# Optimization experiments

Hardware: AMD Instinct MI355X
Metric: run time of the kernel (lower is better)

## Reference

```python
import jax, jax.numpy as jnp
import numpy as np

EMBED = 1024
HEADS = 16
HEAD_DIM = EMBED // HEADS


def setup_inputs() -> dict:
    key = jax.random.key(0)
    ks = jax.random.split(key, 12)
    N, S, E = 4, 2048, EMBED
    scale = 1.0 / np.sqrt(E)
    inp = {
        "values": jax.random.normal(ks[0], (N, S, E), dtype=jnp.float32),
        "keys": jax.random.normal(ks[1], (N, S, E), dtype=jnp.float32),
        "query": jax.random.normal(ks[2], (N, S, E), dtype=jnp.float32),
        "mask": jnp.ones((N, 1, 1, S), dtype=jnp.int32),
        # Linear params: y = x @ W + b (W stored as [in, out])
        "Wv": jax.random.normal(ks[3], (E, E), dtype=jnp.float32) * scale,
        "bv": jnp.zeros((E,), dtype=jnp.float32),
        "Wk": jax.random.normal(ks[4], (E, E), dtype=jnp.float32) * scale,
        "bk": jnp.zeros((E,), dtype=jnp.float32),
        "Wq": jax.random.normal(ks[5], (E, E), dtype=jnp.float32) * scale,
        "bq": jnp.zeros((E,), dtype=jnp.float32),
        "Wo": jax.random.normal(ks[6], (E, E), dtype=jnp.float32) * scale,
        "bo": jnp.zeros((E,), dtype=jnp.float32),
    }
    return inp


def reference(values, keys, query, mask, Wv, bv, Wk, bk, Wq, bq, Wo, bo):
    N, Q, E = query.shape
    V = values.shape[1]
    K = keys.shape[1]
    v = (values @ Wv + bv).reshape(N, V, HEADS, HEAD_DIM)
    k = (keys @ Wk + bk).reshape(N, K, HEADS, HEAD_DIM)
    q = (query @ Wq + bq).reshape(N, Q, HEADS, HEAD_DIM)
    # energy: [N, H, Q, K]
    energy = jnp.einsum("nqhd,nkhd->nhqk", q, k)
    energy = jnp.where(mask == 0, jnp.float32(-1e20), energy)
    # NOTE: original scales by sqrt(embed_size), not sqrt(head_dim)
    attn = jax.nn.softmax(energy / jnp.sqrt(jnp.float32(E)), axis=3)
    out = jnp.einsum("nhql,nlhd->nqhd", attn, v).reshape(N, Q, E)
    return out @ Wo + bo
```

## Files before the change

kernel.cpp:

```cpp
#include <hip/hip_runtime.h>

#define H 16
#define DH 64
#define S 2048
#define E 1024
#define NB 4

typedef short short8_t __attribute__((ext_vector_type(8)));
typedef short short4_t __attribute__((ext_vector_type(4)));
typedef float float4_t __attribute__((ext_vector_type(4)));

__device__ inline unsigned short f2bf(float f) {
    union { float f; unsigned u; } v; v.f = f;
    unsigned r = v.u + 0x7fffu + ((v.u >> 16) & 1u);
    return (unsigned short)(r >> 16);
}

__device__ __forceinline__ unsigned pk_bf16(float a, float b) {
    union { float f; unsigned u; } ua, ub;
    ua.f = a; ub.f = b;
    unsigned ra = ua.u + 0x7fffu + ((ua.u >> 16) & 1u);
    unsigned rb = ub.u + 0x7fffu + ((ub.u >> 16) & 1u);
    return __builtin_amdgcn_perm(rb, ra, 0x07060302u);
}

__device__ __forceinline__ unsigned cvt_pk_bf16(float a, float b) {
    unsigned r;
    asm("v_cvt_pk_bf16_f32 %0, %1, %2" : "=v"(r) : "v"(a), "v"(b));
    return r;
}

__device__ __forceinline__ float4_t mfma16x16x16_bf16(short4_t a, short4_t b, float4_t c) {
#if __has_builtin(__builtin_amdgcn_mfma_f32_16x16x16bf16_1k)
    return __builtin_amdgcn_mfma_f32_16x16x16bf16_1k(a, b, c, 0, 0, 0);
#else
    float4_t d;
    asm("v_mfma_f32_16x16x16_bf16 %0, %1, %2, %3" : "=v"(d) : "v"(a), "v"(b), "v"(c));
    return d;
#endif
}

__device__ __forceinline__ void async_copy16(const unsigned short* g, unsigned short* l) {
    __builtin_amdgcn_global_load_lds(
        (const __attribute__((address_space(1))) unsigned int*)g,
        (__attribute__((address_space(3))) unsigned int*)l, 16, 0, 0);
}

__global__ __launch_bounds__(256) void xcvt_kernel(
    const float* __restrict__ v, const float* __restrict__ k,
    const float* __restrict__ q, unsigned short* __restrict__ xv,
    unsigned short* __restrict__ xk, unsigned short* __restrict__ xq)
{
    const int z = blockIdx.y;
    const float* src = (z == 0) ? v : (z == 1) ? k : q;
    unsigned short* dst = (z == 0) ? xv : (z == 1) ? xk : xq;
    size_t i0 = ((size_t)blockIdx.x * 256 + threadIdx.x) * 8;
    float4 f0 = *reinterpret_cast<const float4*>(src + i0);
    float4 f1 = *reinterpret_cast<const float4*>(src + i0 + 4);
    uint4 o;
    o.x = pk_bf16(f0.x, f0.y); o.y = pk_bf16(f0.z, f0.w);
    o.z = pk_bf16(f1.x, f1.y); o.w = pk_bf16(f1.z, f1.w);
    *reinterpret_cast<uint4*>(dst + i0) = o;
}

__global__ __launch_bounds__(256) void wcvt_kernel(
    const float* __restrict__ Wv, const float* __restrict__ Wk,
    const float* __restrict__ Wq, const float* __restrict__ Wo,
    unsigned short* __restrict__ Wt)
{
    __shared__ float tile[64][65];
    const float* W = (blockIdx.z == 0) ? Wv : (blockIdx.z == 1) ? Wk
                   : (blockIdx.z == 2) ? Wq : Wo;
    unsigned short* out = Wt + (size_t)blockIdx.z * (E * E);
    const int k0 = blockIdx.x * 64, n0 = blockIdx.y * 64;
    const int tid = threadIdx.x;
#pragma unroll
    for (int i = 0; i < 4; ++i) {
        int c = i * 256 + tid;
        int kl = c >> 4, nl4 = (c & 15) * 4;
        float4 v = *reinterpret_cast<const float4*>(W + (size_t)(k0 + kl) * E + n0 + nl4);
        tile[kl][nl4 + 0] = v.x; tile[kl][nl4 + 1] = v.y;
        tile[kl][nl4 + 2] = v.z; tile[kl][nl4 + 3] = v.w;
    }
    __syncthreads();
#pragma unroll
    for (int i = 0; i < 4; ++i) {
        int c = i * 256 + tid;
        int nl = c >> 4, kl4 = (c & 15) * 4;
        ushort4 o;
        o.x = f2bf(tile[kl4 + 0][nl]); o.y = f2bf(tile[kl4 + 1][nl]);
        o.z = f2bf(tile[kl4 + 2][nl]); o.w = f2bf(tile[kl4 + 3][nl]);
        *reinterpret_cast<ushort4*>(out + (size_t)(n0 + nl) * E + k0 + kl4) = o;
    }
}

__global__ __launch_bounds__(256) void proj_kernel(
    const unsigned short* __restrict__ A, const unsigned short* __restrict__ WT,
    const float* __restrict__ bias, unsigned short* __restrict__ out, int mode)
{
    __shared__ __align__(16) unsigned short As[2][128][64];
    __shared__ __align__(16) unsigned short Bs[2][128][64];

    const int tid = threadIdx.x;
    const int m0 = blockIdx.y * 128;
    const int n0 = blockIdx.x * 128;
    const int wave = tid >> 6, lane = tid & 63;
    const int wm = wave >> 1, wn = wave & 1;
    const int quad = lane >> 4, l16 = lane & 15;
    const int r8 = lane >> 3;
    const int c8 = (lane & 7) ^ (r8 & 7);

    float4_t acc[4][4];
#pragma unroll
    for (int i = 0; i < 4; ++i)
#pragma unroll
        for (int j = 0; j < 4; ++j) { float4_t z = {0.f,0.f,0.f,0.f}; acc[i][j] = z; }

#pragma unroll
    for (int j = 0; j < 4; ++j) {
        int row = wave * 32 + j * 8 + r8;
        async_copy16(A  + (size_t)(m0 + row) * E + c8 * 8, &As[0][wave * 32 + j * 8][0]);
        async_copy16(WT + (size_t)(n0 + row) * E + c8 * 8, &Bs[0][wave * 32 + j * 8][0]);
    }

    for (int it = 0; it < 16; ++it) {
        const int cur = it & 1, nxt = cur ^ 1;
        __syncthreads();

        if (it < 15) {
            const int kn = (it + 1) * 64;
#pragma unroll
            for (int j = 0; j < 4; ++j) {
                int row = wave * 32 + j * 8 + r8;
                async_copy16(A  + (size_t)(m0 + row) * E + kn + c8 * 8, &As[nxt][wave * 32 + j * 8][0]);
                async_copy16(WT + (size_t)(n0 + row) * E + kn + c8 * 8, &Bs[nxt][wave * 32 + j * 8][0]);
            }
        }
#pragma unroll
        for (int kk = 0; kk < 2; ++kk) {
            short8_t a[4], b[4];
#pragma unroll
            for (int mi = 0; mi < 4; ++mi)
                a[mi] = *reinterpret_cast<const short8_t*>(
                    &As[cur][wm * 64 + mi * 16 + l16][((kk * 4 + quad) ^ (l16 & 7)) * 8]);
#pragma unroll
            for (int nj = 0; nj < 4; ++nj)
                b[nj] = *reinterpret_cast<const short8_t*>(
                    &Bs[cur][wn * 64 + nj * 16 + l16][((kk * 4 + quad) ^ (l16 & 7)) * 8]);
#pragma unroll
            for (int mi = 0; mi < 4; ++mi)
#pragma unroll
                for (int nj = 0; nj < 4; ++nj)
                    acc[mi][nj] = __builtin_amdgcn_mfma_f32_16x16x32_bf16(a[mi], b[nj], acc[mi][nj], 0, 0, 0);
        }
    }
#pragma unroll
    for (int mi = 0; mi < 4; ++mi) {
#pragma unroll
        for (int nj = 0; nj < 4; ++nj) {
            int gcol = n0 + wn * 64 + nj * 16 + l16;
            float bvv = bias[gcol];
            int h = gcol >> 6, d = gcol & 63;
#pragma unroll
            for (int r = 0; r < 4; ++r) {
                int gm = m0 + wm * 64 + mi * 16 + quad * 4 + r;
                float val = acc[mi][nj][r] + bvv;
                int n = gm >> 11, s = gm & 2047;
                size_t addr;
                if (mode == 0)
                    addr = (((size_t)(n * H + h)) * DH + d) * S + s;
                else
                    addr = (((size_t)(n * H + h)) * S + s) * DH + d;
                out[addr] = f2bf(val);
            }
        }
    }
}

__global__ __launch_bounds__(256, 4) void flash_kernel(
    const unsigned short* __restrict__ Qb, const unsigned short* __restrict__ Kb,
    const unsigned short* __restrict__ VTb, const int* __restrict__ mask,
    unsigned short* __restrict__ AO)
{
    __shared__ __align__(16) unsigned short Ks[2][64][64];
    __shared__ __align__(16) unsigned short Vs[2][64][64];
    __shared__ float am[2][64];
    __shared__ float lbuf[4][32];

    const int tid = threadIdx.x;
    const int wave = tid >> 6, lane = tid & 63;
    const int quad = lane >> 4, l16 = lane & 15;
    const int r8 = lane >> 3;
    const int c8 = (lane & 7) ^ (r8 & 7);

    const int wlin = blockIdx.y * 16 + blockIdx.x;
    const int wid = (wlin & 7) * 128 + (wlin >> 3);
    const int qt = wid & 15;
    const int nh = wid >> 4;
    const int n = nh >> 4, h = nh & 15;
    const size_t hb = (size_t)nh * S * DH;
    const unsigned short* Qh = Qb + hb;
    const unsigned short* Kh = Kb + hb;
    const unsigned short* Vh = VTb + hb;
    const int* mp = mask + n * S;

    const float c1 = 0.03125f * 1.4426950408889634f;
    const float C2_UNMASK = -23.083120654223414f;
    const float C2_MASK   = -1.44e20f;

    short8_t qa[2][2];
#pragma unroll
    for (int qb2 = 0; qb2 < 2; ++qb2)
#pragma unroll
        for (int kk = 0; kk < 2; ++kk) {
            int row = qt * 128 + wave * 32 + qb2 * 16 + l16;
            qa[qb2][kk] = *reinterpret_cast<const short8_t*>(Qh + (size_t)row * DH + kk * 32 + quad * 8);
        }

    float4_t o[2][4];
#pragma unroll
    for (int mi = 0; mi < 2; ++mi)
#pragma unroll
        for (int nj = 0; nj < 4; ++nj) { float4_t z = {0.f,0.f,0.f,0.f}; o[mi][nj] = z; }
    float lsum[2] = {0.f, 0.f};

#pragma unroll
    for (int j = 0; j < 2; ++j) {
        int row = wave * 16 + j * 8 + r8;
        async_copy16(Kh + (size_t)row * DH + c8 * 8, &Ks[0][wave * 16 + j * 8][0]);
        async_copy16(Vh + (size_t)row * S + c8 * 8,  &Vs[0][wave * 16 + j * 8][0]);
    }
    if (tid < 64) am[0][tid] = (mp[tid] == 0) ? C2_MASK : C2_UNMASK;

    for (int it = 0; it < 32; ++it) {
        const int cur = it & 1, nxt = cur ^ 1;
        __syncthreads();

        const int kn = (it < 31) ? (it + 1) * 64 : 0;
#pragma unroll
        for (int j = 0; j < 2; ++j) {
            int row = wave * 16 + j * 8 + r8;
            async_copy16(Kh + (size_t)(kn + row) * DH + c8 * 8, &Ks[nxt][wave * 16 + j * 8][0]);
            async_copy16(Vh + (size_t)row * S + kn + c8 * 8,    &Vs[nxt][wave * 16 + j * 8][0]);
        }
        if (tid < 64) am[nxt][tid] = (mp[kn + tid] == 0) ? C2_MASK : C2_UNMASK;

        float4_t st[4][2];
#pragma unroll
        for (int kvb = 0; kvb < 4; ++kvb)
#pragma unroll
            for (int qb2 = 0; qb2 < 2; ++qb2) { float4_t z = {0.f,0.f,0.f,0.f}; st[kvb][qb2] = z; }
        __builtin_amdgcn_s_setprio(1);
#pragma unroll
        for (int kk = 0; kk < 2; ++kk) {
            short8_t ak[4];
#pragma unroll
            for (int kvb = 0; kvb < 4; ++kvb)
                ak[kvb] = *reinterpret_cast<const short8_t*>(
                    &Ks[cur][kvb * 16 + l16][((kk * 4 + quad) ^ (l16 & 7)) * 8]);
#pragma unroll
            for (int kvb = 0; kvb < 4; ++kvb)
#pragma unroll
                for (int qb2 = 0; qb2 < 2; ++qb2)
                    st[kvb][qb2] = __builtin_amdgcn_mfma_f32_16x16x32_bf16(ak[kvb], qa[qb2][kk], st[kvb][qb2], 0, 0, 0);
        }
        __builtin_amdgcn_s_setprio(0);

        unsigned pw[2][4][2];
#pragma unroll
        for (int kvb = 0; kvb < 4; ++kvb) {
            float4 c2v = *reinterpret_cast<const float4*>(&am[cur][kvb * 16 + quad * 4]);
#pragma unroll
            for (int qb2 = 0; qb2 < 2; ++qb2) {
                float p0 = __builtin_amdgcn_exp2f(st[kvb][qb2][0] * c1 + c2v.x);
                float p1 = __builtin_amdgcn_exp2f(st[kvb][qb2][1] * c1 + c2v.y);
                float p2 = __builtin_amdgcn_exp2f(st[kvb][qb2][2] * c1 + c2v.z);
                float p3 = __builtin_amdgcn_exp2f(st[kvb][qb2][3] * c1 + c2v.w);
                lsum[qb2] += (p0 + p1) + (p2 + p3);
                pw[qb2][kvb][0] = cvt_pk_bf16(p0, p1);
                pw[qb2][kvb][1] = cvt_pk_bf16(p2, p3);
            }
        }

        const int vcol = (quad & 1) * 4;
        __builtin_amdgcn_s_setprio(1);
#pragma unroll
        for (int kvb = 0; kvb < 4; ++kvb) {
            const int vch = ((kvb * 2 + (quad >> 1)) ^ (l16 & 7)) * 8 + vcol;
            short4_t vb[4];
#pragma unroll
            for (int nj = 0; nj < 4; ++nj)
                vb[nj] = *reinterpret_cast<const short4_t*>(&Vs[cur][nj * 16 + l16][vch]);
#pragma unroll
            for (int mi = 0; mi < 2; ++mi) {
                union { unsigned u[2]; short4_t s; } pu;
                pu.u[0] = pw[mi][kvb][0]; pu.u[1] = pw[mi][kvb][1];
#pragma unroll
                for (int nj = 0; nj < 4; ++nj)
                    o[mi][nj] = mfma16x16x16_bf16(pu.s, vb[nj], o[mi][nj]);
            }
        }
        __builtin_amdgcn_s_setprio(0);
    }

    lsum[0] += __shfl_xor(lsum[0], 16); lsum[0] += __shfl_xor(lsum[0], 32);
    lsum[1] += __shfl_xor(lsum[1], 16); lsum[1] += __shfl_xor(lsum[1], 32);
    if (lane < 16) { lbuf[wave][lane] = lsum[0]; lbuf[wave][16 + lane] = lsum[1]; }

#pragma unroll
    for (int mi = 0; mi < 2; ++mi) {
        float4 lv = *reinterpret_cast<const float4*>(&lbuf[wave][mi * 16 + quad * 4]);
#pragma unroll
        for (int r = 0; r < 4; ++r) {
            float invl = __builtin_amdgcn_rcpf(((const float*)&lv)[r]);
            int qrow = qt * 128 + wave * 32 + mi * 16 + quad * 4 + r;
            size_t gm = (size_t)n * S + qrow;
#pragma unroll
            for (int nj = 0; nj < 4; ++nj) {
                int col = h * DH + nj * 16 + l16;
                AO[gm * E + col] = f2bf(o[mi][nj][r] * invl);
            }
        }
    }
}

__global__ __launch_bounds__(256) void ogemm_kernel(
    const unsigned short* __restrict__ A, const unsigned short* __restrict__ WT,
    const float* __restrict__ bias, float* __restrict__ out)
{
    __shared__ __align__(16) unsigned short As[2][128][64];
    __shared__ __align__(16) unsigned short Bs[2][128][64];

    const int tid = threadIdx.x;
    const int m0 = blockIdx.y * 128;
    const int n0 = blockIdx.x * 128;
    const int wave = tid >> 6, lane = tid & 63;
    const int wm = wave >> 1, wn = wave & 1;
    const int quad = lane >> 4, l16 = lane & 15;
    const int r8 = lane >> 3;
    const int c8 = (lane & 7) ^ (r8 & 7);

    float4_t acc[4][4];
#pragma unroll
    for (int i = 0; i < 4; ++i)
#pragma unroll
        for (int j = 0; j < 4; ++j) { float4_t z = {0.f,0.f,0.f,0.f}; acc[i][j] = z; }

#pragma unroll
    for (int j = 0; j < 4; ++j) {
        int row = wave * 32 + j * 8 + r8;
        async_copy16(A  + (size_t)(m0 + row) * E + c8 * 8, &As[0][wave * 32 + j * 8][0]);
        async_copy16(WT + (size_t)(n0 + row) * E + c8 * 8, &Bs[0][wave * 32 + j * 8][0]);
    }

    for (int it = 0; it < 16; ++it) {
        const int cur = it & 1, nxt = cur ^ 1;
        __syncthreads();

        if (it < 15) {
            const int kn = (it + 1) * 64;
#pragma unroll
            for (int j = 0; j < 4; ++j) {
                int row = wave * 32 + j * 8 + r8;
                async_copy16(A  + (size_t)(m0 + row) * E + kn + c8 * 8, &As[nxt][wave * 32 + j * 8][0]);
                async_copy16(WT + (size_t)(n0 + row) * E + kn + c8 * 8, &Bs[nxt][wave * 32 + j * 8][0]);
            }
        }
#pragma unroll
        for (int kk = 0; kk < 2; ++kk) {
            short8_t a[4], b[4];
#pragma unroll
            for (int mi = 0; mi < 4; ++mi)
                a[mi] = *reinterpret_cast<const short8_t*>(
                    &As[cur][wm * 64 + mi * 16 + l16][((kk * 4 + quad) ^ (l16 & 7)) * 8]);
#pragma unroll
            for (int nj = 0; nj < 4; ++nj)
                b[nj] = *reinterpret_cast<const short8_t*>(
                    &Bs[cur][wn * 64 + nj * 16 + l16][((kk * 4 + quad) ^ (l16 & 7)) * 8]);
#pragma unroll
            for (int mi = 0; mi < 4; ++mi)
#pragma unroll
                for (int nj = 0; nj < 4; ++nj)
                    acc[mi][nj] = __builtin_amdgcn_mfma_f32_16x16x32_bf16(a[mi], b[nj], acc[mi][nj], 0, 0, 0);
        }
    }
#pragma unroll
    for (int mi = 0; mi < 4; ++mi)
#pragma unroll
        for (int nj = 0; nj < 4; ++nj) {
            int gcol = n0 + wn * 64 + nj * 16 + l16;
            float bvv = bias[gcol];
#pragma unroll
            for (int r = 0; r < 4; ++r) {
                int gm = m0 + wm * 64 + mi * 16 + quad * 4 + r;
                out[(size_t)gm * E + gcol] = acc[mi][nj][r] + bvv;
            }
        }
}

extern "C" void kernel_launch(void* const* d_in, const int* in_sizes, int n_in,
                              void* d_out, int out_size, void* d_ws, size_t ws_size,
                              hipStream_t stream) {
    const float* values = (const float*)d_in[0];
    const float* keys   = (const float*)d_in[1];
    const float* query  = (const float*)d_in[2];
    const int*   mask   = (const int*)d_in[3];
    const float* Wv = (const float*)d_in[4];  const float* bv = (const float*)d_in[5];
    const float* Wk = (const float*)d_in[6];  const float* bk = (const float*)d_in[7];
    const float* Wq = (const float*)d_in[8];  const float* bq = (const float*)d_in[9];
    const float* Wo = (const float*)d_in[10]; const float* bo = (const float*)d_in[11];
    float* out = (float*)d_out;

    char* ws = (char*)d_ws;
    unsigned short* Wt = (unsigned short*)ws;
    unsigned short* xv = (unsigned short*)(ws + 8388608);
    unsigned short* xk = (unsigned short*)(ws + 25165824);
    unsigned short* xq = (unsigned short*)(ws + 41943040);
    unsigned short* vt = (unsigned short*)(ws + 58720256);
    unsigned short* kb = xv;
    unsigned short* qb = xk;
    unsigned short* ao = xq;

    xcvt_kernel<<<dim3(4096, 3), 256, 0, stream>>>(values, keys, query, xv, xk, xq);
    wcvt_kernel<<<dim3(16, 16, 4), 256, 0, stream>>>(Wv, Wk, Wq, Wo, Wt);
    proj_kernel<<<dim3(8, 64), 256, 0, stream>>>(xv, Wt,           bv, vt, 0);
    proj_kernel<<<dim3(8, 64), 256, 0, stream>>>(xk, Wt + 1048576, bk, kb, 1);
    proj_kernel<<<dim3(8, 64), 256, 0, stream>>>(xq, Wt + 2097152, bq, qb, 1);
    flash_kernel<<<dim3(16, 64), 256, 0, stream>>>(qb, kb, vt, mask, ao);
    ogemm_kernel<<<dim3(8, 64), 256, 0, stream>>>(ao, Wt + 3145728, bo, out);
}
```

Before: 377.4 us.

## Split flash blocks into eight waves and transpose V-projection MFMA for coalesced stores

The flash kernel now runs 512 threads per block. Each wave owns 16 query rows instead of 32, and K and V tile loads are split between the two halves of the block, which lowers per-wave register pressure and raises the number of waves in flight. The projection kernel is templated on mode, and for the V-transpose mode it swaps the MFMA operands so each lane holds consecutive sequence positions, making the transposed output stores more contiguous. In exchange, every K/V shared-memory tile is now reused by more waves, and each MFMA issues with a smaller per-wave tile, which may reduce per-wave compute efficiency.

Result: slower. 401.1 us (+6.3%).

```diff
diff --git a/kernel.cpp b/kernel.cpp
--- a/kernel.cpp
+++ b/kernel.cpp
@@ -94,9 +94,10 @@
     }
 }
 
+template<int MODE>
 __global__ __launch_bounds__(256) void proj_kernel(
     const unsigned short* __restrict__ A, const unsigned short* __restrict__ WT,
-    const float* __restrict__ bias, unsigned short* __restrict__ out, int mode)
+    const float* __restrict__ bias, unsigned short* __restrict__ out)
 {
     __shared__ __align__(16) unsigned short As[2][128][64];
     __shared__ __align__(16) unsigned short Bs[2][128][64];
@@ -148,36 +149,55 @@
                 b[nj] = *reinterpret_cast<const short8_t*>(
                     &Bs[cur][wn * 64 + nj * 16 + l16][((kk * 4 + quad) ^ (l16 & 7)) * 8]);
 #pragma unroll
-            for (int mi = 0; mi < 4; ++mi)
-#pragma unroll
-                for (int nj = 0; nj < 4; ++nj)
-                    acc[mi][nj] = __builtin_amdgcn_mfma_f32_16x16x32_bf16(a[mi], b[nj], acc[mi][nj], 0, 0, 0);
-        }
-    }
-#pragma unroll
-    for (int mi = 0; mi < 4; ++mi) {
-#pragma unroll
-        for (int nj = 0; nj < 4; ++nj) {
-            int gcol = n0 + wn * 64 + nj * 16 + l16;
-            float bvv = bias[gcol];
-            int h = gcol >> 6, d = gcol & 63;
-#pragma unroll
-            for (int r = 0; r < 4; ++r) {
-                int gm = m0 + wm * 64 + mi * 16 + quad * 4 + r;
-                float val = acc[mi][nj][r] + bvv;
-                int n = gm >> 11, s = gm & 2047;
-                size_t addr;
-                if (mode == 0)
-                    addr = (((size_t)(n * H + h)) * DH + d) * S + s;
-                else
-                    addr = (((size_t)(n * H + h)) * S + s) * DH + d;
-                out[addr] = f2bf(val);
+            for (int x = 0; x < 4; ++x)
+#pragma unroll
+                for (int y = 0; y < 4; ++y) {
+                    if (MODE == 0)
+                        acc[x][y] = __builtin_amdgcn_mfma_f32_16x16x32_bf16(b[x], a[y], acc[x][y], 0, 0, 0);
+                    else
+                        acc[x][y] = __builtin_amdgcn_mfma_f32_16x16x32_bf16(a[x], b[y], acc[x][y], 0, 0, 0);
+                }
+        }
+    }
+
+    if (MODE == 0) {
+#pragma unroll
+        for (int x = 0; x < 4; ++x) {
+            float4 bb = *reinterpret_cast<const float4*>(&bias[n0 + wn * 64 + x * 16 + quad * 4]);
+#pragma unroll
+            for (int y = 0; y < 4; ++y) {
+                int m = m0 + wm * 64 + y * 16 + l16;
+                int nn = m >> 11, s = m & 2047;
+#pragma unroll
+                for (int r = 0; r < 4; ++r) {
+                    int gcol = n0 + wn * 64 + x * 16 + quad * 4 + r;
+                    int h = gcol >> 6, d = gcol & 63;
+                    float val = acc[x][y][r] + ((const float*)&bb)[r];
+                    out[(((size_t)(nn * H + h)) * DH + d) * S + s] = f2bf(val);
+                }
             }
         }
-    }
-}
-
-__global__ __launch_bounds__(256, 4) void flash_kernel(
+    } else {
+#pragma unroll
+        for (int x = 0; x < 4; ++x) {
+#pragma unroll
+            for (int y = 0; y < 4; ++y) {
+                int gcol = n0 + wn * 64 + y * 16 + l16;
+                float bvv = bias[gcol];
+                int h = gcol >> 6, d = gcol & 63;
+#pragma unroll
+                for (int r = 0; r < 4; ++r) {
+                    int gm = m0 + wm * 64 + x * 16 + quad * 4 + r;
+                    float val = acc[x][y][r] + bvv;
+                    int nn = gm >> 11, s = gm & 2047;
+                    out[(((size_t)(nn * H + h)) * S + s) * DH + d] = f2bf(val);
+                }
+            }
+        }
+    }
+}
+
+__global__ __launch_bounds__(512, 8) void flash_kernel(
     const unsigned short* __restrict__ Qb, const unsigned short* __restrict__ Kb,
     const unsigned short* __restrict__ VTb, const int* __restrict__ mask,
     unsigned short* __restrict__ AO)
@@ -185,13 +205,14 @@
     __shared__ __align__(16) unsigned short Ks[2][64][64];
     __shared__ __align__(16) unsigned short Vs[2][64][64];
     __shared__ float am[2][64];
-    __shared__ float lbuf[4][32];
+    __shared__ float lbuf[8][16];
 
     const int tid = threadIdx.x;
     const int wave = tid >> 6, lane = tid & 63;
     const int quad = lane >> 4, l16 = lane & 15;
     const int r8 = lane >> 3;
     const int c8 = (lane & 7) ^ (r8 & 7);
+    const int sw = wave & 3;
 
     const int wlin = blockIdx.y * 16 + blockIdx.x;
     const int wid = (wlin & 7) * 128 + (wlin >> 3);
@@ -208,27 +229,23 @@
     const float C2_UNMASK = -23.083120654223414f;
     const float C2_MASK   = -1.44e20f;
 
-    short8_t qa[2][2];
-#pragma unroll
-    for (int qb2 = 0; qb2 < 2; ++qb2)
-#pragma unroll
-        for (int kk = 0; kk < 2; ++kk) {
-            int row = qt * 128 + wave * 32 + qb2 * 16 + l16;
-            qa[qb2][kk] = *reinterpret_cast<const short8_t*>(Qh + (size_t)row * DH + kk * 32 + quad * 8);
-        }
-
-    float4_t o[2][4];
-#pragma unroll
-    for (int mi = 0; mi < 2; ++mi)
-#pragma unroll
-        for (int nj = 0; nj < 4; ++nj) { float4_t z = {0.f,0.f,0.f,0.f}; o[mi][nj] = z; }
-    float lsum[2] = {0.f, 0.f};
+    short8_t qa[2];
+#pragma unroll
+    for (int kk = 0; kk < 2; ++kk) {
+        int row = qt * 128 + wave * 16 + l16;
+        qa[kk] = *reinterpret_cast<const short8_t*>(Qh + (size_t)row * DH + kk * 32 + quad * 8);
+    }
+
+    float4_t o[4];
+#pragma unroll
+    for (int nj = 0; nj < 4; ++nj) { float4_t z = {0.f,0.f,0.f,0.f}; o[nj] = z; }
+    float lsum = 0.f;
 
 #pragma unroll
     for (int j = 0; j < 2; ++j) {
-        int row = wave * 16 + j * 8 + r8;
-        async_copy16(Kh + (size_t)row * DH + c8 * 8, &Ks[0][wave * 16 + j * 8][0]);
-        async_copy16(Vh + (size_t)row * S + c8 * 8,  &Vs[0][wave * 16 + j * 8][0]);
+        int row = sw * 16 + j * 8 + r8;
+        if (wave < 4) async_copy16(Kh + (size_t)row * DH + c8 * 8, &Ks[0][sw * 16 + j * 8][0]);
+        else          async_copy16(Vh + (size_t)row * S + c8 * 8,  &Vs[0][sw * 16 + j * 8][0]);
     }
     if (tid < 64) am[0][tid] = (mp[tid] == 0) ? C2_MASK : C2_UNMASK;
 
@@ -239,17 +256,15 @@
         const int kn = (it < 31) ? (it + 1) * 64 : 0;
 #pragma unroll
         for (int j = 0; j < 2; ++j) {
-            int row = wave * 16 + j * 8 + r8;
-            async_copy16(Kh + (size_t)(kn + row) * DH + c8 * 8, &Ks[nxt][wave * 16 + j * 8][0]);
-            async_copy16(Vh + (size_t)row * S + kn + c8 * 8,    &Vs[nxt][wave * 16 + j * 8][0]);
+            int row = sw * 16 + j * 8 + r8;
+            if (wave < 4) async_copy16(Kh + (size_t)(kn + row) * DH + c8 * 8, &Ks[nxt][sw * 16 + j * 8][0]);
+            else          async_copy16(Vh + (size_t)row * S + kn + c8 * 8,    &Vs[nxt][sw * 16 + j * 8][0]);
         }
         if (tid < 64) am[nxt][tid] = (mp[kn + tid] == 0) ? C2_MASK : C2_UNMASK;
 
-        float4_t st[4][2];
-#pragma unroll
-        for (int kvb = 0; kvb < 4; ++kvb)
-#pragma unroll
-            for (int qb2 = 0; qb2 < 2; ++qb2) { float4_t z = {0.f,0.f,0.f,0.f}; st[kvb][qb2] = z; }
+        float4_t st[4];
+#pragma unroll
+        for (int kvb = 0; kvb < 4; ++kvb) { float4_t z = {0.f,0.f,0.f,0.f}; st[kvb] = z; }
         __builtin_amdgcn_s_setprio(1);
 #pragma unroll
         for (int kk = 0; kk < 2; ++kk) {
@@ -260,26 +275,21 @@
                     &Ks[cur][kvb * 16 + l16][((kk * 4 + quad) ^ (l16 & 7)) * 8]);
 #pragma unroll
             for (int kvb = 0; kvb < 4; ++kvb)
-#pragma unroll
-                for (int qb2 = 0; qb2 < 2; ++qb2)
-                    st[kvb][qb2] = __builtin_amdgcn_mfma_f32_16x16x32_bf16(ak[kvb], qa[qb2][kk], st[kvb][qb2], 0, 0, 0);
+                st[kvb] = __builtin_amdgcn_mfma_f32_16x16x32_bf16(ak[kvb], qa[kk], st[kvb], 0, 0, 0);
         }
         __builtin_amdgcn_s_setprio(0);
 
-        unsigned pw[2][4][2];
+        unsigned pw[4][2];
 #pragma unroll
         for (int kvb = 0; kvb < 4; ++kvb) {
             float4 c2v = *reinterpret_cast<const float4*>(&am[cur][kvb * 16 + quad * 4]);
-#pragma unroll
-            for (int qb2 = 0; qb2 < 2; ++qb2) {
-                float p0 = __builtin_amdgcn_exp2f(st[kvb][qb2][0] * c1 + c2v.x);
-                float p1 = __builtin_amdgcn_exp2f(st[kvb][qb2][1] * c1 + c2v.y);
-                float p2 = __builtin_amdgcn_exp2f(st[kvb][qb2][2] * c1 + c2v.z);
-                float p3 = __builtin_amdgcn_exp2f(st[kvb][qb2][3] * c1 + c2v.w);
-                lsum[qb2] += (p0 + p1) + (p2 + p3);
-                pw[qb2][kvb][0] = cvt_pk_bf16(p0, p1);
-                pw[qb2][kvb][1] = cvt_pk_bf16(p2, p3);
-            }
+            float p0 = __builtin_amdgcn_exp2f(st[kvb][0] * c1 + c2v.x);
+            float p1 = __builtin_amdgcn_exp2f(st[kvb][1] * c1 + c2v.y);
+            float p2 = __builtin_amdgcn_exp2f(st[kvb][2] * c1 + c2v.z);
+            float p3 = __builtin_amdgcn_exp2f(st[kvb][3] * c1 + c2v.w);
+            lsum += (p0 + p1) + (p2 + p3);
+            pw[kvb][0] = cvt_pk_bf16(p0, p1);
+            pw[kvb][1] = cvt_pk_bf16(p2, p3);
         }
 
         const int vcol = (quad & 1) * 4;
@@ -291,35 +301,28 @@
 #pragma unroll
             for (int nj = 0; nj < 4; ++nj)
                 vb[nj] = *reinterpret_cast<const short4_t*>(&Vs[cur][nj * 16 + l16][vch]);
-#pragma unroll
-            for (int mi = 0; mi < 2; ++mi) {
-                union { unsigned u[2]; short4_t s; } pu;
-                pu.u[0] = pw[mi][kvb][0]; pu.u[1] = pw[mi][kvb][1];
-#pragma unroll
-                for (int nj = 0; nj < 4; ++nj)
-                    o[mi][nj] = mfma16x16x16_bf16(pu.s, vb[nj], o[mi][nj]);
-            }
+            union { unsigned u[2]; short4_t s; } pu;
+            pu.u[0] = pw[kvb][0]; pu.u[1] = pw[kvb][1];
+#pragma unroll
+            for (int nj = 0; nj < 4; ++nj)
+                o[nj] = mfma16x16x16_bf16(pu.s, vb[nj], o[nj]);
         }
         __builtin_amdgcn_s_setprio(0);
     }
 
-    lsum[0] += __shfl_xor(lsum[0], 16); lsum[0] += __shfl_xor(lsum[0], 32);
-    lsum[1] += __shfl_xor(lsum[1], 16); lsum[1] += __shfl_xor(lsum[1], 32);
-    if (lane < 16) { lbuf[wave][lane] = lsum[0]; lbuf[wave][16 + lane] = lsum[1]; }
-
-#pragma unroll
-    for (int mi = 0; mi < 2; ++mi) {
-        float4 lv = *reinterpret_cast<const float4*>(&lbuf[wave][mi * 16 + quad * 4]);
-#pragma unroll
-        for (int r = 0; r < 4; ++r) {
-            float invl = __builtin_amdgcn_rcpf(((const float*)&lv)[r]);
-            int qrow = qt * 128 + wave * 32 + mi * 16 + quad * 4 + r;
-            size_t gm = (size_t)n * S + qrow;
-#pragma unroll
-            for (int nj = 0; nj < 4; ++nj) {
-                int col = h * DH + nj * 16 + l16;
-                AO[gm * E + col] = f2bf(o[mi][nj][r] * invl);
-            }
+    lsum += __shfl_xor(lsum, 16); lsum += __shfl_xor(lsum, 32);
+    if (lane < 16) lbuf[wave][lane] = lsum;
+
+    float4 lv = *reinterpret_cast<const float4*>(&lbuf[wave][quad * 4]);
+#pragma unroll
+    for (int r = 0; r < 4; ++r) {
+        float invl = __builtin_amdgcn_rcpf(((const float*)&lv)[r]);
+        int qrow = qt * 128 + wave * 16 + quad * 4 + r;
+        size_t gm = (size_t)n * S + qrow;
+#pragma unroll
+        for (int nj = 0; nj < 4; ++nj) {
+            int col = h * DH + nj * 16 + l16;
+            AO[gm * E + col] = f2bf(o[nj][r] * invl);
         }
     }
 }
@@ -423,9 +426,9 @@
 
     xcvt_kernel<<<dim3(4096, 3), 256, 0, stream>>>(values, keys, query, xv, xk, xq);
     wcvt_kernel<<<dim3(16, 16, 4), 256, 0, stream>>>(Wv, Wk, Wq, Wo, Wt);
-    proj_kernel<<<dim3(8, 64), 256, 0, stream>>>(xv, Wt,           bv, vt, 0);
-    proj_kernel<<<dim3(8, 64), 256, 0, stream>>>(xk, Wt + 1048576, bk, kb, 1);
-    proj_kernel<<<dim3(8, 64), 256, 0, stream>>>(xq, Wt + 2097152, bq, qb, 1);
-    flash_kernel<<<dim3(16, 64), 256, 0, stream>>>(qb, kb, vt, mask, ao);
+    proj_kernel<0><<<dim3(8, 64), 256, 0, stream>>>(xv, Wt,           bv, vt);
+    proj_kernel<1><<<dim3(8, 64), 256, 0, stream>>>(xk, Wt + 1048576, bk, kb);
+    proj_kernel<1><<<dim3(8, 64), 256, 0, stream>>>(xq, Wt + 2097152, bq, qb);
+    flash_kernel<<<dim3(16, 64), 512, 0, stream>>>(qb, kb, vt, mask, ao);
     ogemm_kernel<<<dim3(8, 64), 256, 0, stream>>>(ao, Wt + 3145728, bo, out);
 }
```
